# Kernel tuning notes

Hardware: AMD Instinct MI355X
Metric: run time of the kernel (lower is better)

## Reference

```python
import math
import jax, jax.numpy as jnp
import numpy as np

D_MODEL = 2048
HEAD = 128
DEPTH = 12
LAMBDA_INIT = 0.8 - 0.6 * math.exp(-0.3 * DEPTH)
RMS_EPS = float(np.finfo(np.float32).eps)  # torch RMSNorm default eps=None -> finfo.eps


def setup_inputs() -> dict:
    key = jax.random.key(0)
    ks = jax.random.split(key, 9)
    B, S = 2, 4096
    std_l = 0.1
    return {
        "x": jax.random.normal(ks[0], (B, S, D_MODEL), dtype=jnp.float32),
        "Wq": jax.random.normal(ks[1], (HEAD, D_MODEL), dtype=jnp.float32) / math.sqrt(D_MODEL),
        "Wk": jax.random.normal(ks[2], (HEAD, D_MODEL), dtype=jnp.float32) / math.sqrt(D_MODEL),
        "Wv": jax.random.normal(ks[3], (HEAD, D_MODEL), dtype=jnp.float32) / math.sqrt(D_MODEL),
        "lambda_q1": std_l * jax.random.normal(ks[4], (HEAD // 2,), dtype=jnp.float32),
        "lambda_q2": std_l * jax.random.normal(ks[5], (HEAD // 2,), dtype=jnp.float32),
        "lambda_k1": std_l * jax.random.normal(ks[6], (HEAD // 2,), dtype=jnp.float32),
        "lambda_k2": std_l * jax.random.normal(ks[7], (HEAD // 2,), dtype=jnp.float32),
        "rms_weight": jnp.ones((HEAD,), dtype=jnp.float32),
    }


def reference(x, Wq, Wk, Wv, lambda_q1, lambda_q2, lambda_k1, lambda_k2, rms_weight):
    # projections (torch Linear: x @ W.T)
    q = jnp.einsum("bsd,hd->bsh", x, Wq)
    k = jnp.einsum("bsd,hd->bsh", x, Wk)
    v = jnp.einsum("bsd,hd->bsh", x, Wv)
    h2 = HEAD // 2
    q1, q2 = q[..., :h2], q[..., h2:]
    k1, k2 = k[..., :h2], k[..., h2:]
    scale = 1.0 / math.sqrt(h2)
    attn1 = jax.nn.softmax(jnp.einsum("bqh,bkh->bqk", q1, k1) * scale, axis=-1)
    attn2 = jax.nn.softmax(jnp.einsum("bqh,bkh->bqk", q2, k2) * scale, axis=-1)
    lam = jnp.exp(jnp.dot(lambda_q1, lambda_k1)) - jnp.exp(jnp.dot(lambda_q2, lambda_k2)) + LAMBDA_INIT
    attn_out = jnp.einsum("bqk,bkh->bqh", attn1 - lam * attn2, v)
    # RMSNorm over last dim
    rms = jax.lax.rsqrt(jnp.mean(attn_out * attn_out, axis=-1, keepdims=True) + RMS_EPS)
    return (1.0 - LAMBDA_INIT) * (attn_out * rms * rms_weight)
```

## Files before the change

### kernel.cpp

```cpp
#include <hip/hip_runtime.h>
#include <hip/hip_bf16.h>
#include <math.h>

#define S_LEN 4096
#define DMODEL 2048
#define HEADD 128

typedef __attribute__((ext_vector_type(8))) short short8;
typedef __attribute__((ext_vector_type(4))) float floatx4;

__device__ __forceinline__ short f2bs(float f) {
  __hip_bfloat16 h = __float2bfloat16(f);
  short s; __builtin_memcpy(&s, &h, 2); return s;
}
__device__ __forceinline__ float bs2f(short s) {
  unsigned u = ((unsigned)(unsigned short)s) << 16;
  float f; __builtin_memcpy(&f, &u, 4); return f;
}
__device__ __forceinline__ int pkbf(float a, float b) {
  return (int)(((unsigned)(unsigned short)f2bs(b) << 16) |
               (unsigned)(unsigned short)f2bs(a));
}
__device__ __forceinline__ float fexp2(float x) { return __builtin_amdgcn_exp2f(x); }
__device__ __forceinline__ void gl_lds16(const short* g, short* l) {
  __builtin_amdgcn_global_load_lds(
      (const __attribute__((address_space(1))) unsigned int*)(g),
      (__attribute__((address_space(3))) unsigned int*)(l), 16, 0, 0);
}

__global__ __launch_bounds__(256) void convw_kernel(const float* __restrict__ wq,
                                                    const float* __restrict__ wk,
                                                    const float* __restrict__ wv,
                                                    short* __restrict__ wc) {
  const int per = 128 * 2048;
  int e = (blockIdx.x * blockDim.x + threadIdx.x) * 4;
  const float* src = (e < per) ? wq : (e < 2 * per) ? wk : wv;
  int off = e & (per - 1);
  float4 v = *(const float4*)(src + off);
  short4 r;
  r.x = f2bs(v.x); r.y = f2bs(v.y); r.z = f2bs(v.z); r.w = f2bs(v.w);
  *(short4*)(wc + e) = r;
}

__global__ __launch_bounds__(256, 4) void proj_kernel(const float* __restrict__ x,
                                                      const short* __restrict__ wc,
                                                      short* __restrict__ qa0,
                                                      short* __restrict__ qa1) {
  const int tid = threadIdx.x;
  const int w = tid >> 6;
  const int lane = tid & 63;
  const int lo = lane & 15, g = lane >> 4;
  const int id = blockIdx.x;
  const int kh = id >> 9, nq = (id >> 7) & 3, mb = id & 127;
  const int m0 = mb * 64;
  const int n0 = nq * 96;
  const int k0 = kh * 1024;
  short* qa = kh ? qa1 : qa0;

  __shared__ short xt[2][64 * 64];
  __shared__ short wt[2][96 * 64];

  const int r8 = tid >> 3, sc = tid & 7;
  const float* xs0 = x + (size_t)(m0 + r8) * DMODEL + k0 + sc * 8;
  const float* xs1 = x + (size_t)(m0 + 32 + r8) * DMODEL + k0 + sc * 8;
  const int xl0 = r8 * 64 + ((sc ^ (r8 & 7)) * 8);
  const int xl1 = (32 + r8) * 64 + ((sc ^ (r8 & 7)) * 8);

  const short* wg[3];
  int wdo[3];
#pragma unroll
  for (int j = 0; j < 3; ++j) {
    int ci = w * 192 + j * 64 + lane;
    int r = ci >> 3, cs = ci & 7;
    int csrc = cs ^ (r & 7);
    wg[j] = wc + (size_t)(n0 + r) * DMODEL + k0 + csrc * 8;
    wdo[j] = (w * 192 + j * 64) * 8;
  }

  const int mrow = (w >> 1) * 32;
  const int ncol = (w & 1) * 48;
  int aoff[2][2], boff[3][2];
#pragma unroll
  for (int mi = 0; mi < 2; ++mi) {
    int r = mrow + mi * 16 + lo;
#pragma unroll
    for (int kc = 0; kc < 2; ++kc)
      aoff[mi][kc] = r * 64 + (((kc * 4 + g) ^ (r & 7)) * 8);
  }
#pragma unroll
  for (int t = 0; t < 3; ++t) {
    int r = ncol + t * 16 + lo;
#pragma unroll
    for (int kc = 0; kc < 2; ++kc)
      boff[t][kc] = r * 64 + (((kc * 4 + g) ^ (r & 7)) * 8);
  }

  floatx4 acc[2][3];
#pragma unroll
  for (int mi = 0; mi < 2; ++mi)
#pragma unroll
    for (int t = 0; t < 3; ++t) acc[mi][t] = floatx4{0.f, 0.f, 0.f, 0.f};

  {
#pragma unroll
    for (int j = 0; j < 3; ++j) gl_lds16(wg[j], &wt[0][wdo[j]]);
    float4 a0 = *(const float4*)(xs0), a1 = *(const float4*)(xs0 + 4);
    float4 b0 = *(const float4*)(xs1), b1 = *(const float4*)(xs1 + 4);
    short8 sA, sB;
    sA[0]=f2bs(a0.x); sA[1]=f2bs(a0.y); sA[2]=f2bs(a0.z); sA[3]=f2bs(a0.w);
    sA[4]=f2bs(a1.x); sA[5]=f2bs(a1.y); sA[6]=f2bs(a1.z); sA[7]=f2bs(a1.w);
    sB[0]=f2bs(b0.x); sB[1]=f2bs(b0.y); sB[2]=f2bs(b0.z); sB[3]=f2bs(b0.w);
    sB[4]=f2bs(b1.x); sB[5]=f2bs(b1.y); sB[6]=f2bs(b1.z); sB[7]=f2bs(b1.w);
    *(short8*)&xt[0][xl0] = sA;
    *(short8*)&xt[0][xl1] = sB;
  }
  __syncthreads();

  int cur = 0;
#pragma unroll 1
  for (int it = 0; it < 16; ++it) {
    float4 a0, a1, b0, b1;
    if (it + 1 < 16) {
      const int k = (it + 1) * 64;
#pragma unroll
      for (int j = 0; j < 3; ++j) gl_lds16(wg[j] + k, &wt[cur ^ 1][wdo[j]]);
      a0 = *(const float4*)(xs0 + k); a1 = *(const float4*)(xs0 + k + 4);
      b0 = *(const float4*)(xs1 + k); b1 = *(const float4*)(xs1 + k + 4);
    }

    {
      const short* xb = &xt[cur][0];
      const short* wb = &wt[cur][0];
      short8 af[2][2], bf[3][2];
#pragma unroll
      for (int mi = 0; mi < 2; ++mi)
#pragma unroll
        for (int kc = 0; kc < 2; ++kc) af[mi][kc] = *(const short8*)(xb + aoff[mi][kc]);
#pragma unroll
      for (int t = 0; t < 3; ++t)
#pragma unroll
        for (int kc = 0; kc < 2; ++kc) bf[t][kc] = *(const short8*)(wb + boff[t][kc]);
#pragma unroll
      for (int kc = 0; kc < 2; ++kc)
#pragma unroll
        for (int mi = 0; mi < 2; ++mi)
#pragma unroll
          for (int t = 0; t < 3; ++t)
            acc[mi][t] = __builtin_amdgcn_mfma_f32_16x16x32_bf16(af[mi][kc], bf[t][kc], acc[mi][t], 0, 0, 0);
    }

    if (it + 1 < 16) {
      short8 sA, sB;
      sA[0]=f2bs(a0.x); sA[1]=f2bs(a0.y); sA[2]=f2bs(a0.z); sA[3]=f2bs(a0.w);
      sA[4]=f2bs(a1.x); sA[5]=f2bs(a1.y); sA[6]=f2bs(a1.z); sA[7]=f2bs(a1.w);
      sB[0]=f2bs(b0.x); sB[1]=f2bs(b0.y); sB[2]=f2bs(b0.z); sB[3]=f2bs(b0.w);
      sB[4]=f2bs(b1.x); sB[5]=f2bs(b1.y); sB[6]=f2bs(b1.z); sB[7]=f2bs(b1.w);
      *(short8*)&xt[cur ^ 1][xl0] = sA;
      *(short8*)&xt[cur ^ 1][xl1] = sB;
    }
    __syncthreads();
    cur ^= 1;
  }

#pragma unroll
  for (int t = 0; t < 3; ++t) {
    int n = n0 + ncol + t * 16 + lo;
#pragma unroll
    for (int mi = 0; mi < 2; ++mi)
#pragma unroll
      for (int j = 0; j < 4; ++j) {
        int m = m0 + mrow + mi * 16 + g * 4 + j;
        qa[(size_t)m * 384 + n] = f2bs(acc[mi][t][j]);
      }
  }
}

__global__ __launch_bounds__(256) void conv_qk_kernel(const short* __restrict__ qa0,
                                                      const short* __restrict__ qa1,
                                                      short* __restrict__ qm,
                                                      short* __restrict__ kb) {
  int e = (blockIdx.x * 256 + threadIdx.x) * 4;
  int m = e >> 8, c = e & 255;
  short4 a = *(const short4*)(qa0 + (size_t)m * 384 + c);
  short4 b = *(const short4*)(qa1 + (size_t)m * 384 + c);
  float vx = bs2f(a.x) + bs2f(b.x);
  float vy = bs2f(a.y) + bs2f(b.y);
  float vz = bs2f(a.z) + bs2f(b.z);
  float vw = bs2f(a.w) + bs2f(b.w);
  short4 r;
  if (c < 128) {
    const float sc = 0.18033688011112042f;
    r.x = f2bs(vx * sc); r.y = f2bs(vy * sc);
    r.z = f2bs(vz * sc); r.w = f2bs(vw * sc);
    *(short4*)(qm + (size_t)m * 128 + c) = r;
  } else {
    r.x = f2bs(vx); r.y = f2bs(vy); r.z = f2bs(vz); r.w = f2bs(vw);
    *(short4*)(kb + (size_t)m * 128 + (c - 128)) = r;
  }
}

__global__ __launch_bounds__(256) void conv_v_kernel(const short* __restrict__ qa0,
                                                     const short* __restrict__ qa1,
                                                     short* __restrict__ vt) {
  const int tid = threadIdx.x;
  const int bb = blockIdx.x >> 6, st = blockIdx.x & 63;
  const int s0 = st * 64;

  __shared__ short ld[64][136];

  const int r = tid >> 2, c8 = (tid & 3) * 32;
#pragma unroll
  for (int q = 0; q < 4; ++q) {
    const size_t off = (size_t)(bb * 4096 + s0 + r) * 384 + 256 + c8 + q * 8;
    short8 a = *(const short8*)(qa0 + off);
    short8 b = *(const short8*)(qa1 + off);
    short8 o;
#pragma unroll
    for (int i = 0; i < 8; ++i) o[i] = f2bs(bs2f(a[i]) + bs2f(b[i]));
    *(short8*)(&ld[r][c8 + q * 8]) = o;
  }
  __syncthreads();

  const int h = tid >> 1, sh = (tid & 1) * 32;
#pragma unroll
  for (int q = 0; q < 4; ++q) {
    short8 t;
#pragma unroll
    for (int i = 0; i < 8; ++i) {
      int src5 = (i < 4) ? (4 * q + i) : (16 + 4 * q + (i - 4));
      t[i] = ld[sh + src5][h];
    }
    *(short8*)(vt + ((size_t)bb * 128 + h) * 4096 + s0 + sh + q * 8) = t;
  }
}

__global__ __launch_bounds__(256, 3) void attn_kernel(const short* __restrict__ qm,
                                                      const short* __restrict__ kb,
                                                      const short* __restrict__ vt,
                                                      short* __restrict__ po,
                                                      float* __restrict__ pls) {
  const int tid = threadIdx.x;
  const int w = tid >> 6;
  const int lane = tid & 63;
  const int lo = lane & 15, g = lane >> 4;
  const int qsp = w >> 1;
  const int s = w & 1;
  const int id = blockIdx.x;
  const int ksp = id & 7;
  const int qblk = id >> 3;
  const int b = qblk >> 6;
  const int kv_base = ksp * 512;

  __shared__ short kt[2][32 * 128];
  __shared__ short vl[2][128 * 32];

  const short* kS = kb + (size_t)b * S_LEN * HEADD;
  const short* vS = vt + (size_t)b * HEADD * S_LEN;

  const short* kg[2];
  const short* vg[2];
  int kdo[2], vdo[2];
#pragma unroll
  for (int j = 0; j < 2; ++j) {
    int ci = w * 128 + j * 64 + lane;
    int kr = ci >> 4, kcs = (ci & 15) ^ (kr & 7);
    kg[j] = kS + (size_t)(kv_base + kr) * HEADD + kcs * 8;
    kdo[j] = (w * 128 + j * 64) * 8;
    int vr = ci >> 2, vcs = (ci & 3) ^ (vr & 3);
    vg[j] = vS + (size_t)vr * S_LEN + kv_base + vcs * 8;
    vdo[j] = (w * 128 + j * 64) * 8;
  }

  const int rowqA = qblk * 64 + qsp * 32;
  const int rowqB = rowqA + 16;
  const short* qrowA = qm + (size_t)(rowqA + lo) * HEADD + s * 64;
  const short* qrowB = qm + (size_t)(rowqB + lo) * HEADD + s * 64;
  const short8 qA0 = *(const short8*)(qrowA + g * 8);
  const short8 qA1 = *(const short8*)(qrowA + 32 + g * 8);
  const short8 qB0 = *(const short8*)(qrowB + g * 8);
  const short8 qB1 = *(const short8*)(qrowB + 32 + g * 8);

  floatx4 accA[8], accB[8];
#pragma unroll
  for (int n = 0; n < 8; ++n) {
    accA[n] = floatx4{0.f, 0.f, 0.f, 0.f};
    accB[n] = floatx4{0.f, 0.f, 0.f, 0.f};
  }
  floatx4 lxA = floatx4{0.f, 0.f, 0.f, 0.f};
  floatx4 lxB = floatx4{0.f, 0.f, 0.f, 0.f};

  short8 onesb;
  {
    short one = (short)0x3F80;
#pragma unroll
    for (int jj = 0; jj < 8; ++jj) onesb[jj] = (lo == 0) ? one : (short)0;
  }

  const int kc0 = ((s * 8 + g) ^ (lo & 7)) * 8;
  const int kc1 = ((s * 8 + 4 + g) ^ (lo & 7)) * 8;
  const int kro0 = lo * 128, kro1 = (16 + lo) * 128;
  const int vco = (g ^ (lo & 3)) * 8;

#pragma unroll
  for (int j = 0; j < 2; ++j) {
    gl_lds16(kg[j], &kt[0][kdo[j]]);
    gl_lds16(vg[j], &vl[0][vdo[j]]);
  }
  __syncthreads();

  int cur = 0;
#pragma unroll 1
  for (int it = 0; it < 16; ++it) {
    if (it + 1 < 16) {
      const int ko = (it + 1) * 32 * HEADD;
      const int vo = (it + 1) * 32;
#pragma unroll
      for (int j = 0; j < 2; ++j) {
        gl_lds16(kg[j] + ko, &kt[cur ^ 1][kdo[j]]);
        gl_lds16(vg[j] + vo, &vl[cur ^ 1][vdo[j]]);
      }
    }

    const short* kbase = &kt[cur][0];
    short8 a00 = *(const short8*)(kbase + kro0 + kc0);
    short8 a01 = *(const short8*)(kbase + kro0 + kc1);
    short8 a10 = *(const short8*)(kbase + kro1 + kc0);
    short8 a11 = *(const short8*)(kbase + kro1 + kc1);

    floatx4 z = floatx4{0.f, 0.f, 0.f, 0.f};
    floatx4 u;
    u = __builtin_amdgcn_mfma_f32_16x16x32_bf16(a00, qA0, z, 0, 0, 0);
    floatx4 T0A = __builtin_amdgcn_mfma_f32_16x16x32_bf16(a01, qA1, u, 0, 0, 0);
    u = __builtin_amdgcn_mfma_f32_16x16x32_bf16(a10, qA0, z, 0, 0, 0);
    floatx4 T1A = __builtin_amdgcn_mfma_f32_16x16x32_bf16(a11, qA1, u, 0, 0, 0);
    u = __builtin_amdgcn_mfma_f32_16x16x32_bf16(a00, qB0, z, 0, 0, 0);
    floatx4 T0B = __builtin_amdgcn_mfma_f32_16x16x32_bf16(a01, qB1, u, 0, 0, 0);
    u = __builtin_amdgcn_mfma_f32_16x16x32_bf16(a10, qB0, z, 0, 0, 0);
    floatx4 T1B = __builtin_amdgcn_mfma_f32_16x16x32_bf16(a11, qB1, u, 0, 0, 0);

    short8 paA, paB;
    {
      float p0 = fexp2(T0A[0]), p1 = fexp2(T0A[1]), p2 = fexp2(T0A[2]), p3 = fexp2(T0A[3]);
      float p4 = fexp2(T1A[0]), p5 = fexp2(T1A[1]), p6 = fexp2(T1A[2]), p7 = fexp2(T1A[3]);
      int4 tmp = {pkbf(p0, p1), pkbf(p2, p3), pkbf(p4, p5), pkbf(p6, p7)};
      __builtin_memcpy(&paA, &tmp, 16);
    }
    {
      float p0 = fexp2(T0B[0]), p1 = fexp2(T0B[1]), p2 = fexp2(T0B[2]), p3 = fexp2(T0B[3]);
      float p4 = fexp2(T1B[0]), p5 = fexp2(T1B[1]), p6 = fexp2(T1B[2]), p7 = fexp2(T1B[3]);
      int4 tmp = {pkbf(p0, p1), pkbf(p2, p3), pkbf(p4, p5), pkbf(p6, p7)};
      __builtin_memcpy(&paB, &tmp, 16);
    }

    const short* vbase = &vl[cur][0];
#pragma unroll
    for (int n = 0; n < 8; ++n) {
      short8 vf = *(const short8*)(vbase + (n * 16 + lo) * 32 + vco);
      accA[n] = __builtin_amdgcn_mfma_f32_16x16x32_bf16(paA, vf, accA[n], 0, 0, 0);
      accB[n] = __builtin_amdgcn_mfma_f32_16x16x32_bf16(paB, vf, accB[n], 0, 0, 0);
    }
    lxA = __builtin_amdgcn_mfma_f32_16x16x32_bf16(paA, onesb, lxA, 0, 0, 0);
    lxB = __builtin_amdgcn_mfma_f32_16x16x32_bf16(paB, onesb, lxB, 0, 0, 0);

    __syncthreads();
    cur ^= 1;
  }

  short* pw = po + ((size_t)(ksp * 2 + s) * 8192) * 128;
#pragma unroll
  for (int j = 0; j < 4; ++j) {
    short8 pk;
#pragma unroll
    for (int n = 0; n < 8; ++n) pk[n] = f2bs(accA[n][j]);
    *(short8*)(pw + (size_t)(rowqA + g * 4 + j) * 128 + lo * 8) = pk;
#pragma unroll
    for (int n = 0; n < 8; ++n) pk[n] = f2bs(accB[n][j]);
    *(short8*)(pw + (size_t)(rowqB + g * 4 + j) * 128 + lo * 8) = pk;
  }
  if (lo == 0) {
#pragma unroll
    for (int j = 0; j < 4; ++j) {
      pls[(size_t)(ksp * 2 + s) * 8192 + rowqA + g * 4 + j] = lxA[j];
      pls[(size_t)(ksp * 2 + s) * 8192 + rowqB + g * 4 + j] = lxB[j];
    }
  }
}

__global__ __launch_bounds__(256) void merge_kernel(const short* __restrict__ po,
                                                    const float* __restrict__ pls,
                                                    const float* __restrict__ lq1,
                                                    const float* __restrict__ lq2,
                                                    const float* __restrict__ lk1,
                                                    const float* __restrict__ lk2,
                                                    const float* __restrict__ rmsw,
                                                    float* __restrict__ out) {
  const int tid = threadIdx.x;
  const int row = blockIdx.x * 16 + (tid >> 4);
  const int lo = tid & 15;

  float a1s = 0.f, a2s = 0.f;
  for (int i = 0; i < 64; ++i) {
    a1s = fmaf(lq1[i], lk1[i], a1s);
    a2s = fmaf(lq2[i], lk2[i], a2s);
  }
  const float lam = __expf(a1s) - __expf(a2s) + 0.7836057665316245f;

  float o1[8], o2[8];
#pragma unroll
  for (int n = 0; n < 8; ++n) { o1[n] = 0.f; o2[n] = 0.f; }
  float l1 = 0.f, l2 = 0.f;
#pragma unroll
  for (int ksp = 0; ksp < 8; ++ksp) {
    short8 sa = *(const short8*)(po + ((size_t)(ksp * 2 + 0) * 8192 + row) * 128 + lo * 8);
    short8 sb = *(const short8*)(po + ((size_t)(ksp * 2 + 1) * 8192 + row) * 128 + lo * 8);
#pragma unroll
    for (int n = 0; n < 8; ++n) { o1[n] += bs2f(sa[n]); o2[n] += bs2f(sb[n]); }
    l1 += pls[(size_t)(ksp * 2 + 0) * 8192 + row];
    l2 += pls[(size_t)(ksp * 2 + 1) * 8192 + row];
  }
  const float iL1 = 1.f / l1, iL2 = 1.f / l2;

  float v[8];
  float ssq = 0.f;
#pragma unroll
  for (int n = 0; n < 8; ++n) {
    v[n] = o1[n] * iL1 - lam * (o2[n] * iL2);
    ssq += v[n] * v[n];
  }
  ssq += __shfl_xor(ssq, 1);
  ssq += __shfl_xor(ssq, 2);
  ssq += __shfl_xor(ssq, 4);
  ssq += __shfl_xor(ssq, 8);
  const float rr = rsqrtf(ssq * (1.f / 128.f) + 1.1920928955078125e-07f);

  float* ob = out + (size_t)row * 128;
#pragma unroll
  for (int n = 0; n < 8; ++n) {
    int c = n * 16 + lo;
    ob[c] = 0.21639423346837554f * v[n] * rr * rmsw[c];
  }
}

extern "C" void kernel_launch(void* const* d_in, const int* in_sizes, int n_in,
                              void* d_out, int out_size, void* d_ws, size_t ws_size,
                              hipStream_t stream) {
  const float* x   = (const float*)d_in[0];
  const float* wq  = (const float*)d_in[1];
  const float* wk  = (const float*)d_in[2];
  const float* wv  = (const float*)d_in[3];
  const float* lq1 = (const float*)d_in[4];
  const float* lq2 = (const float*)d_in[5];
  const float* lk1 = (const float*)d_in[6];
  const float* lk2 = (const float*)d_in[7];
  const float* rw  = (const float*)d_in[8];
  float* out = (float*)d_out;

  char* ws = (char*)d_ws;
  short* qm  = (short*)(ws);
  short* kb  = (short*)(ws + (2u << 20));
  short* vt  = (short*)(ws + (4u << 20));
  short* wc  = (short*)(ws + (6u << 20));
  short* qa0 = (short*)(ws + (8u << 20));
  short* qa1 = (short*)(ws + (8u << 20) + 6291456u);
  short* po  = (short*)(ws + (8u << 20));
  float* pls = (float*)(ws + (40u << 20));

  convw_kernel<<<768, 256, 0, stream>>>(wq, wk, wv, wc);
  proj_kernel<<<1024, 256, 0, stream>>>(x, wc, qa0, qa1);
  conv_qk_kernel<<<2048, 256, 0, stream>>>(qa0, qa1, qm, kb);
  conv_v_kernel<<<128, 256, 0, stream>>>(qa0, qa1, vt);
  attn_kernel<<<1024, 256, 0, stream>>>(qm, kb, vt, po, pls);
  merge_kernel<<<512, 256, 0, stream>>>(po, pls, lq1, lq2, lk1, lk2, rw, out);
}
```

Before: 90.58 us.

## Load projection operands directly into registers and remap blocks per XCD

The projection GEMM no longer stages x and weight tiles through shared memory with double buffering and barriers. Each wave now loads its MFMA fragments straight from global memory, converting x to bf16 in registers. Block IDs are also remapped so consecutive M blocks land on the same XCD, which should improve L2 reuse of x rows. In exchange, each x and weight element is read by more waves (two waves share each A and B fragment), and without the prefetch there is less latency hiding.

After: 163.1 us. 1.8x slower.

```diff
diff --git a/kernel.cpp b/kernel.cpp
--- a/kernel.cpp
+++ b/kernel.cpp
@@ -51,49 +51,23 @@
   const int lane = tid & 63;
   const int lo = lane & 15, g = lane >> 4;
   const int id = blockIdx.x;
-  const int kh = id >> 9, nq = (id >> 7) & 3, mb = id & 127;
+  const int xcd = id & 7, loc = id >> 3;
+  const int mb = xcd * 16 + (loc & 15);
+  const int sh = loc >> 4;
+  const int nq = sh & 3, kh = sh >> 2;
   const int m0 = mb * 64;
   const int n0 = nq * 96;
   const int k0 = kh * 1024;
   short* qa = kh ? qa1 : qa0;
 
-  __shared__ short xt[2][64 * 64];
-  __shared__ short wt[2][96 * 64];
-
-  const int r8 = tid >> 3, sc = tid & 7;
-  const float* xs0 = x + (size_t)(m0 + r8) * DMODEL + k0 + sc * 8;
-  const float* xs1 = x + (size_t)(m0 + 32 + r8) * DMODEL + k0 + sc * 8;
-  const int xl0 = r8 * 64 + ((sc ^ (r8 & 7)) * 8);
-  const int xl1 = (32 + r8) * 64 + ((sc ^ (r8 & 7)) * 8);
-
-  const short* wg[3];
-  int wdo[3];
-#pragma unroll
-  for (int j = 0; j < 3; ++j) {
-    int ci = w * 192 + j * 64 + lane;
-    int r = ci >> 3, cs = ci & 7;
-    int csrc = cs ^ (r & 7);
-    wg[j] = wc + (size_t)(n0 + r) * DMODEL + k0 + csrc * 8;
-    wdo[j] = (w * 192 + j * 64) * 8;
-  }
-
   const int mrow = (w >> 1) * 32;
   const int ncol = (w & 1) * 48;
-  int aoff[2][2], boff[3][2];
-#pragma unroll
-  for (int mi = 0; mi < 2; ++mi) {
-    int r = mrow + mi * 16 + lo;
-#pragma unroll
-    for (int kc = 0; kc < 2; ++kc)
-      aoff[mi][kc] = r * 64 + (((kc * 4 + g) ^ (r & 7)) * 8);
-  }
-#pragma unroll
-  for (int t = 0; t < 3; ++t) {
-    int r = ncol + t * 16 + lo;
-#pragma unroll
-    for (int kc = 0; kc < 2; ++kc)
-      boff[t][kc] = r * 64 + (((kc * 4 + g) ^ (r & 7)) * 8);
-  }
+
+  const float* xA0 = x + (size_t)(m0 + mrow + lo) * DMODEL + k0 + g * 8;
+  const float* xA1 = x + (size_t)(m0 + mrow + 16 + lo) * DMODEL + k0 + g * 8;
+  const short* wB0 = wc + (size_t)(n0 + ncol + lo) * DMODEL + k0 + g * 8;
+  const short* wB1 = wc + (size_t)(n0 + ncol + 16 + lo) * DMODEL + k0 + g * 8;
+  const short* wB2 = wc + (size_t)(n0 + ncol + 32 + lo) * DMODEL + k0 + g * 8;
 
   floatx4 acc[2][3];
 #pragma unroll
@@ -101,65 +75,54 @@
 #pragma unroll
     for (int t = 0; t < 3; ++t) acc[mi][t] = floatx4{0.f, 0.f, 0.f, 0.f};
 
-  {
-#pragma unroll
-    for (int j = 0; j < 3; ++j) gl_lds16(wg[j], &wt[0][wdo[j]]);
-    float4 a0 = *(const float4*)(xs0), a1 = *(const float4*)(xs0 + 4);
-    float4 b0 = *(const float4*)(xs1), b1 = *(const float4*)(xs1 + 4);
-    short8 sA, sB;
-    sA[0]=f2bs(a0.x); sA[1]=f2bs(a0.y); sA[2]=f2bs(a0.z); sA[3]=f2bs(a0.w);
-    sA[4]=f2bs(a1.x); sA[5]=f2bs(a1.y); sA[6]=f2bs(a1.z); sA[7]=f2bs(a1.w);
-    sB[0]=f2bs(b0.x); sB[1]=f2bs(b0.y); sB[2]=f2bs(b0.z); sB[3]=f2bs(b0.w);
-    sB[4]=f2bs(b1.x); sB[5]=f2bs(b1.y); sB[6]=f2bs(b1.z); sB[7]=f2bs(b1.w);
-    *(short8*)&xt[0][xl0] = sA;
-    *(short8*)&xt[0][xl1] = sB;
-  }
-  __syncthreads();
-
-  int cur = 0;
 #pragma unroll 1
   for (int it = 0; it < 16; ++it) {
-    float4 a0, a1, b0, b1;
-    if (it + 1 < 16) {
-      const int k = (it + 1) * 64;
-#pragma unroll
-      for (int j = 0; j < 3; ++j) gl_lds16(wg[j] + k, &wt[cur ^ 1][wdo[j]]);
-      a0 = *(const float4*)(xs0 + k); a1 = *(const float4*)(xs0 + k + 4);
-      b0 = *(const float4*)(xs1 + k); b1 = *(const float4*)(xs1 + k + 4);
-    }
-
-    {
-      const short* xb = &xt[cur][0];
-      const short* wb = &wt[cur][0];
-      short8 af[2][2], bf[3][2];
-#pragma unroll
-      for (int mi = 0; mi < 2; ++mi)
-#pragma unroll
-        for (int kc = 0; kc < 2; ++kc) af[mi][kc] = *(const short8*)(xb + aoff[mi][kc]);
-#pragma unroll
-      for (int t = 0; t < 3; ++t)
-#pragma unroll
-        for (int kc = 0; kc < 2; ++kc) bf[t][kc] = *(const short8*)(wb + boff[t][kc]);
-#pragma unroll
-      for (int kc = 0; kc < 2; ++kc)
-#pragma unroll
-        for (int mi = 0; mi < 2; ++mi)
-#pragma unroll
-          for (int t = 0; t < 3; ++t)
-            acc[mi][t] = __builtin_amdgcn_mfma_f32_16x16x32_bf16(af[mi][kc], bf[t][kc], acc[mi][t], 0, 0, 0);
-    }
-
-    if (it + 1 < 16) {
-      short8 sA, sB;
-      sA[0]=f2bs(a0.x); sA[1]=f2bs(a0.y); sA[2]=f2bs(a0.z); sA[3]=f2bs(a0.w);
-      sA[4]=f2bs(a1.x); sA[5]=f2bs(a1.y); sA[6]=f2bs(a1.z); sA[7]=f2bs(a1.w);
-      sB[0]=f2bs(b0.x); sB[1]=f2bs(b0.y); sB[2]=f2bs(b0.z); sB[3]=f2bs(b0.w);
-      sB[4]=f2bs(b1.x); sB[5]=f2bs(b1.y); sB[6]=f2bs(b1.z); sB[7]=f2bs(b1.w);
-      *(short8*)&xt[cur ^ 1][xl0] = sA;
-      *(short8*)&xt[cur ^ 1][xl1] = sB;
-    }
-    __syncthreads();
-    cur ^= 1;
+    const int kb = it * 64;
+
+    float4 a00 = *(const float4*)(xA0 + kb);
+    float4 a01 = *(const float4*)(xA0 + kb + 4);
+    float4 a02 = *(const float4*)(xA0 + kb + 32);
+    float4 a03 = *(const float4*)(xA0 + kb + 36);
+    float4 a10 = *(const float4*)(xA1 + kb);
+    float4 a11 = *(const float4*)(xA1 + kb + 4);
+    float4 a12 = *(const float4*)(xA1 + kb + 32);
+    float4 a13 = *(const float4*)(xA1 + kb + 36);
+    short8 b00 = *(const short8*)(wB0 + kb);
+    short8 b01 = *(const short8*)(wB0 + kb + 32);
+    short8 b10 = *(const short8*)(wB1 + kb);
+    short8 b11 = *(const short8*)(wB1 + kb + 32);
+    short8 b20 = *(const short8*)(wB2 + kb);
+    short8 b21 = *(const short8*)(wB2 + kb + 32);
+
+    short8 af[2][2];
+#pragma unroll
+    for (int q = 0; q < 2; ++q) {
+      const float4& u0 = q ? a10 : a00;
+      const float4& u1 = q ? a11 : a01;
+      const float4& u2 = q ? a12 : a02;
+      const float4& u3 = q ? a13 : a03;
+      af[q][0][0] = f2bs(u0.x); af[q][0][1] = f2bs(u0.y);
+      af[q][0][2] = f2bs(u0.z); af[q][0][3] = f2bs(u0.w);
+      af[q][0][4] = f2bs(u1.x); af[q][0][5] = f2bs(u1.y);
+      af[q][0][6] = f2bs(u1.z); af[q][0][7] = f2bs(u1.w);
+      af[q][1][0] = f2bs(u2.x); af[q][1][1] = f2bs(u2.y);
+      af[q][1][2] = f2bs(u2.z); af[q][1][3] = f2bs(u2.w);
+      af[q][1][4] = f2bs(u3.x); af[q][1][5] = f2bs(u3.y);
+      af[q][1][6] = f2bs(u3.z); af[q][1][7] = f2bs(u3.w);
+    }
+
+    acc[0][0] = __builtin_amdgcn_mfma_f32_16x16x32_bf16(af[0][0], b00, acc[0][0], 0, 0, 0);
+    acc[0][1] = __builtin_amdgcn_mfma_f32_16x16x32_bf16(af[0][0], b10, acc[0][1], 0, 0, 0);
+    acc[0][2] = __builtin_amdgcn_mfma_f32_16x16x32_bf16(af[0][0], b20, acc[0][2], 0, 0, 0);
+    acc[1][0] = __builtin_amdgcn_mfma_f32_16x16x32_bf16(af[1][0], b00, acc[1][0], 0, 0, 0);
+    acc[1][1] = __builtin_amdgcn_mfma_f32_16x16x32_bf16(af[1][0], b10, acc[1][1], 0, 0, 0);
+    acc[1][2] = __builtin_amdgcn_mfma_f32_16x16x32_bf16(af[1][0], b20, acc[1][2], 0, 0, 0);
+    acc[0][0] = __builtin_amdgcn_mfma_f32_16x16x32_bf16(af[0][1], b01, acc[0][0], 0, 0, 0);
+    acc[0][1] = __builtin_amdgcn_mfma_f32_16x16x32_bf16(af[0][1], b11, acc[0][1], 0, 0, 0);
+    acc[0][2] = __builtin_amdgcn_mfma_f32_16x16x32_bf16(af[0][1], b21, acc[0][2], 0, 0, 0);
+    acc[1][0] = __builtin_amdgcn_mfma_f32_16x16x32_bf16(af[1][1], b01, acc[1][0], 0, 0, 0);
+    acc[1][1] = __builtin_amdgcn_mfma_f32_16x16x32_bf16(af[1][1], b11, acc[1][1], 0, 0, 0);
+    acc[1][2] = __builtin_amdgcn_mfma_f32_16x16x32_bf16(af[1][1], b21, acc[1][2], 0, 0, 0);
   }
 
 #pragma unroll
```
